# Optimization experiments

Hardware: AMD Instinct MI355X
Metric: run time of the kernel (lower is better)

Reference implementation:

```python
import jax, jax.numpy as jnp
import numpy as np


def setup_inputs() -> dict:
    key = jax.random.key(0)
    k1, k2, k3 = jax.random.split(key, 3)
    bs, seqlen, hidden = 2, 2048, 1024
    s, h = 4, 256  # sqrt_n_heads, head_size
    std = 0.02
    num_layers = 12
    hidden_states = jax.random.normal(k1, (bs, seqlen, hidden), dtype=jnp.float32)
    q_scale = 1.0 / np.sqrt(2.0 * num_layers * h)
    queries = jax.random.normal(k2, (s, h, h * s), dtype=jnp.float32) * std * q_scale
    combiners = jax.random.normal(k3, (s, h * s, h), dtype=jnp.float32) * (std * q_scale)
    return {"hidden_states": hidden_states, "queries": queries, "combiners": combiners}


def reference(hidden_states, queries, combiners):
    # queries: [s1, h, s*h], combiners: [s1, s*h, h]
    s, h, _ = queries.shape
    bs, S, E = hidden_states.shape
    x = hidden_states.reshape(bs, S, s, h)            # [b, t, s, h]
    qw = queries.reshape(s, h, s, h)                  # [s1, h_in, s2, h_out]
    # projected queries, already permuted to [s2, b, t, s1, f]
    Q = jnp.einsum('btae,aeqf->qbtaf', x, qw)
    # pre-attention scores: [s2, b, t, s1, u] (u = key position)  ~O(S^2)
    pre = jnp.einsum('qbtaf,buqf->qbtau', Q, x)
    # attention output, permuted to [s1, b, t, s2, g]
    attn = jnp.einsum('qbtau,buqg->abtqg', pre, x)
    attn = attn.reshape(s, bs, S, s * h)              # [s1, b, t, s2*h]
    out = jnp.einsum('abtk,akg->btag', attn, combiners)
    return out.reshape(bs, S, s * h)
```

## Files before the change

### kernel.cpp

```cpp
#include <hip/hip_runtime.h>
#include <hip/hip_bf16.h>


typedef unsigned short u16;
using short8  = __attribute__((ext_vector_type(8))) short;
using floatx4 = __attribute__((ext_vector_type(4))) float;

__device__ inline u16 f2bf(float f) {
    unsigned u = __float_as_uint(f);
    unsigned r = u + 0x7fffu + ((u >> 16) & 1u);
    return (u16)(r >> 16);
}

template <typename T>
__device__ inline void stage64(const T* __restrict__ src, long ld,
                               u16* __restrict__ dst, int tid) {
#pragma unroll
    for (int it = 0; it < 4; ++it) {
        const int flat = (it * 256 + tid) * 4;
        const int kl = flat & 63, rl = flat >> 6;
        ushort4 v;
        if (sizeof(T) == 4) {
            const float4 f = *(const float4*)&((const float*)src)[(long)rl * ld + kl];
            v.x = f2bf(f.x); v.y = f2bf(f.y); v.z = f2bf(f.z); v.w = f2bf(f.w);
        } else {
            v = *(const ushort4*)&((const u16*)src)[(long)rl * ld + kl];
        }
        const int chunk = ((kl >> 5) * 4 + (rl >> 4)) * 64 + ((kl >> 3) & 3) * 16 + (rl & 15);
        *(ushort4*)&dst[chunk * 8 + (kl & 7)] = v;
    }
}

__device__ inline void stage_km64(const float* __restrict__ src, long ld,
                                  u16* __restrict__ dst, int tid) {
#pragma unroll
    for (int it = 0; it < 4; ++it) {
        const int flat = (it * 256 + tid) * 4;
        const int m = flat & 63, k = flat >> 6;
        const float4 f = *(const float4*)&src[(long)k * ld + m];
        const int cb_ = ((k >> 5) * 4 + (m >> 4)) * 64 + ((k & 31) >> 3) * 16 + (m & 15);
        const int j = k & 7;
        dst[(cb_ + 0) * 8 + j] = f2bf(f.x);
        dst[(cb_ + 1) * 8 + j] = f2bf(f.y);
        dst[(cb_ + 2) * 8 + j] = f2bf(f.z);
        dst[(cb_ + 3) * 8 + j] = f2bf(f.w);
    }
}

template <typename TA, typename TB, bool AKM, bool BKM, bool ATOMIC>
__device__ inline void gemm_tile(const TA* __restrict__ A, long lda,
                                 const TB* __restrict__ B, long ldb,
                                 float* __restrict__ C, long ldc,
                                 int m0, int n0) {
    __shared__ u16 As[16384];
    __shared__ u16 Bs[16384];
    const int tid = threadIdx.x, lane = tid & 63, w = tid >> 6;
    const int IA = (w & 1) * 2, JB = (w >> 1) * 2;
    floatx4 acc[2][2] = {};

#pragma unroll
    for (int kb = 0; kb < 4; ++kb) {
        if (AKM) stage_km64((const float*)A + (long)(kb * 64) * lda, lda, As + kb * 4096, tid);
        else     stage64(A + kb * 64, lda, As + kb * 4096, tid);
    }
#pragma unroll
    for (int kb = 0; kb < 4; ++kb) {
        if (BKM) stage_km64((const float*)B + (long)(kb * 64) * ldb, ldb, Bs + kb * 4096, tid);
        else     stage64(B + kb * 64, ldb, Bs + kb * 4096, tid);
    }
    __syncthreads();

#pragma unroll
    for (int kb = 0; kb < 4; ++kb)
#pragma unroll
        for (int s = 0; s < 2; ++s) {
            short8 af[2], bfr[2];
#pragma unroll
            for (int i = 0; i < 2; ++i)
                af[i] = *(const short8*)&As[kb * 4096 + ((s * 4 + IA + i) * 64 + lane) * 8];
#pragma unroll
            for (int j = 0; j < 2; ++j)
                bfr[j] = *(const short8*)&Bs[kb * 4096 + ((s * 4 + JB + j) * 64 + lane) * 8];
#pragma unroll
            for (int i = 0; i < 2; ++i)
#pragma unroll
                for (int j = 0; j < 2; ++j)
                    acc[i][j] = __builtin_amdgcn_mfma_f32_16x16x32_bf16(af[i], bfr[j], acc[i][j], 0, 0, 0);
        }

    const int rb = (lane >> 4) * 4, col = lane & 15;
#pragma unroll
    for (int i = 0; i < 2; ++i)
#pragma unroll
        for (int j = 0; j < 2; ++j)
#pragma unroll
            for (int r = 0; r < 4; ++r) {
                const int gm = m0 + (IA + i) * 16 + rb + r;
                const int gn = n0 + (JB + j) * 16 + col;
                float* p = &C[(long)gm * ldc + gn];
                if (ATOMIC) atomicAdd(p, acc[i][j][r]); else *p = acc[i][j][r];
            }
}

__global__ __launch_bounds__(256) void k_gram(const float* __restrict__ x,
                                              float* __restrict__ G) {
    const int tile = blockIdx.x, bq = blockIdx.y, split = blockIdx.z;
    const int tm = tile >> 2, tn = tile & 3;
    const int b = bq >> 2, q = bq & 3;
    const float* base = x + (long)b * 2097152 + (long)split * 256 * 1024 + q * 256;
    gemm_tile<float, float, true, true, true>(
        base + tm * 64, 1024,
        base + tn * 64, 1024,
        G + (long)bq * 65536, 256,
        tm * 64, tn * 64);
}

__global__ __launch_bounds__(256) void k_2a(const float* __restrict__ comb,
                                            const float* __restrict__ G,
                                            float* __restrict__ Tt) {
    const int tile = blockIdx.x, i = blockIdx.y;
    const int tm = tile >> 2, tn = tile & 3;
    const int q = i & 3, ba = i >> 2, b = ba >> 2, a = ba & 3;
    gemm_tile<float, float, true, false, false>(
        comb + (long)a * 262144 + (long)q * 256 * 256 + tm * 64, 256,
        G + (long)(b * 4 + q) * 65536 + (long)tn * 64 * 256, 256,
        Tt + (long)ba * 262144, 1024,
        tm * 64, q * 256 + tn * 64);
}

__global__ __launch_bounds__(256) void k_2b(const float* __restrict__ Tt,
                                            const float* __restrict__ qw,
                                            float* __restrict__ Wt) {
    const int tile = blockIdx.x, ba = blockIdx.y, split = blockIdx.z;
    const int tm = tile >> 2, tn = tile & 3;
    const int a = ba & 3;
    gemm_tile<float, float, false, false, true>(
        Tt + (long)ba * 262144 + (long)tm * 64 * 1024 + split * 256, 1024,
        qw + (long)a * 262144 + (long)tn * 64 * 1024 + split * 256, 1024,
        Wt + (long)ba * 65536, 256,
        tm * 64, tn * 64);
}

__global__ __launch_bounds__(256) void k_3(const float* __restrict__ x,
                                           const float* __restrict__ Wt,
                                           float* __restrict__ out) {
    const int tl = blockIdx.x, ba = blockIdx.y;
    const int tm = tl >> 2, tn = tl & 3;
    const int b = ba >> 2, a = ba & 3;
    gemm_tile<float, float, false, false, false>(
        x + (long)b * 2097152 + (long)tm * 64 * 1024 + a * 256, 1024,
        Wt + (long)ba * 65536 + (long)tn * 64 * 256, 256,
        out + (long)b * 2097152 + a * 256, 1024,
        tm * 64, tn * 64);
}

extern "C" void kernel_launch(void* const* d_in, const int* in_sizes, int n_in,
                              void* d_out, int out_size, void* d_ws, size_t ws_size,
                              hipStream_t stream) {
    const float* x    = (const float*)d_in[0];
    const float* qw   = (const float*)d_in[1];
    const float* comb = (const float*)d_in[2];
    float* out = (float*)d_out;

    char* ws = (char*)d_ws;
    float* G  = (float*)(ws);
    float* Wt = (float*)(ws + (2u << 20));
    float* Tt = (float*)(ws + (4u << 20));

    hipMemsetAsync(d_ws, 0, 4u << 20, stream);
    k_gram<<<dim3(16, 8, 8), 256, 0, stream>>>(x, G);
    k_2a  <<<dim3(16, 32),   256, 0, stream>>>(comb, G, Tt);
    k_2b  <<<dim3(16, 8, 4), 256, 0, stream>>>(Tt, qw, Wt);
    k_3   <<<dim3(128, 8),   256, 0, stream>>>(x, Wt, out);
}
```

Baseline: 140.4 us.

## Replace atomic split-K Gram with partial buffers, fold zeroing, store Tt as bf16

The Gram kernel now writes per-split partial results to separate buffers instead of accumulating them with atomics. The next kernel sums the eight partials while staging its B operand. The separate memset is removed: the Gram kernel zeroes the Wt accumulator itself. Tt is stored as bf16, which halves its write and read traffic, at the cost of 8x more Gram partial storage and extra reads in k_2a.

```diff
diff --git a/kernel.cpp b/kernel.cpp
--- a/kernel.cpp
+++ b/kernel.cpp
@@ -26,6 +26,27 @@
         } else {
             v = *(const ushort4*)&((const u16*)src)[(long)rl * ld + kl];
         }
+        const int chunk = ((kl >> 5) * 4 + (rl >> 4)) * 64 + ((kl >> 3) & 3) * 16 + (rl & 15);
+        *(ushort4*)&dst[chunk * 8 + (kl & 7)] = v;
+    }
+}
+
+__device__ inline void stage64_sum8(const float* __restrict__ s0, long ld,
+                                    long partStride,
+                                    u16* __restrict__ dst, int tid) {
+#pragma unroll
+    for (int it = 0; it < 4; ++it) {
+        const int flat = (it * 256 + tid) * 4;
+        const int kl = flat & 63, rl = flat >> 6;
+        const long off = (long)rl * ld + kl;
+        float4 acc = *(const float4*)&s0[off];
+#pragma unroll
+        for (int s = 1; s < 8; ++s) {
+            const float4 f = *(const float4*)&s0[(long)s * partStride + off];
+            acc.x += f.x; acc.y += f.y; acc.z += f.z; acc.w += f.w;
+        }
+        ushort4 v;
+        v.x = f2bf(acc.x); v.y = f2bf(acc.y); v.z = f2bf(acc.z); v.w = f2bf(acc.w);
         const int chunk = ((kl >> 5) * 4 + (rl >> 4)) * 64 + ((kl >> 3) & 3) * 16 + (rl & 15);
         *(ushort4*)&dst[chunk * 8 + (kl & 7)] = v;
     }
@@ -47,10 +68,12 @@
     }
 }
 
-template <typename TA, typename TB, bool AKM, bool BKM, bool ATOMIC>
+template <typename TA, typename TB, typename TC,
+          bool AKM, bool BKM, bool BSUM8, bool ATOMIC>
 __device__ inline void gemm_tile(const TA* __restrict__ A, long lda,
                                  const TB* __restrict__ B, long ldb,
-                                 float* __restrict__ C, long ldc,
+                                 long partStride,
+                                 TC* __restrict__ C, long ldc,
                                  int m0, int n0) {
     __shared__ u16 As[16384];
     __shared__ u16 Bs[16384];
@@ -65,8 +88,9 @@
     }
 #pragma unroll
     for (int kb = 0; kb < 4; ++kb) {
-        if (BKM) stage_km64((const float*)B + (long)(kb * 64) * ldb, ldb, Bs + kb * 4096, tid);
-        else     stage64(B + kb * 64, ldb, Bs + kb * 4096, tid);
+        if (BSUM8)    stage64_sum8((const float*)B + kb * 64, ldb, partStride, Bs + kb * 4096, tid);
+        else if (BKM) stage_km64((const float*)B + (long)(kb * 64) * ldb, ldb, Bs + kb * 4096, tid);
+        else          stage64(B + kb * 64, ldb, Bs + kb * 4096, tid);
     }
     __syncthreads();
 
@@ -97,46 +121,57 @@
             for (int r = 0; r < 4; ++r) {
                 const int gm = m0 + (IA + i) * 16 + rb + r;
                 const int gn = n0 + (JB + j) * 16 + col;
-                float* p = &C[(long)gm * ldc + gn];
-                if (ATOMIC) atomicAdd(p, acc[i][j][r]); else *p = acc[i][j][r];
+                TC* p = &C[(long)gm * ldc + gn];
+                if (sizeof(TC) == 2) *(u16*)p = f2bf(acc[i][j][r]);
+                else if (ATOMIC) atomicAdd((float*)p, acc[i][j][r]);
+                else *(float*)p = acc[i][j][r];
             }
 }
 
 __global__ __launch_bounds__(256) void k_gram(const float* __restrict__ x,
-                                              float* __restrict__ G) {
+                                              float* __restrict__ Gp,
+                                              float* __restrict__ Wt) {
     const int tile = blockIdx.x, bq = blockIdx.y, split = blockIdx.z;
     const int tm = tile >> 2, tn = tile & 3;
     const int b = bq >> 2, q = bq & 3;
+    {
+        const int bl = tile + 16 * bq + 128 * split;
+        if (threadIdx.x < 128) {
+            const float4 zero = {0.f, 0.f, 0.f, 0.f};
+            ((float4*)(Wt + (long)bl * 512))[threadIdx.x] = zero;
+        }
+    }
     const float* base = x + (long)b * 2097152 + (long)split * 256 * 1024 + q * 256;
-    gemm_tile<float, float, true, true, true>(
+    gemm_tile<float, float, float, true, true, false, false>(
         base + tm * 64, 1024,
-        base + tn * 64, 1024,
-        G + (long)bq * 65536, 256,
+        base + tn * 64, 1024, 0,
+        Gp + (long)(split * 8 + bq) * 65536, 256,
         tm * 64, tn * 64);
 }
 
 __global__ __launch_bounds__(256) void k_2a(const float* __restrict__ comb,
-                                            const float* __restrict__ G,
-                                            float* __restrict__ Tt) {
+                                            const float* __restrict__ Gp,
+                                            u16* __restrict__ Tt) {
     const int tile = blockIdx.x, i = blockIdx.y;
     const int tm = tile >> 2, tn = tile & 3;
     const int q = i & 3, ba = i >> 2, b = ba >> 2, a = ba & 3;
-    gemm_tile<float, float, true, false, false>(
+    gemm_tile<float, float, u16, true, false, true, false>(
         comb + (long)a * 262144 + (long)q * 256 * 256 + tm * 64, 256,
-        G + (long)(b * 4 + q) * 65536 + (long)tn * 64 * 256, 256,
+        Gp + (long)(b * 4 + q) * 65536 + (long)tn * 64 * 256, 256,
+        (long)8 * 65536,
         Tt + (long)ba * 262144, 1024,
         tm * 64, q * 256 + tn * 64);
 }
 
-__global__ __launch_bounds__(256) void k_2b(const float* __restrict__ Tt,
+__global__ __launch_bounds__(256) void k_2b(const u16* __restrict__ Tt,
                                             const float* __restrict__ qw,
                                             float* __restrict__ Wt) {
     const int tile = blockIdx.x, ba = blockIdx.y, split = blockIdx.z;
     const int tm = tile >> 2, tn = tile & 3;
     const int a = ba & 3;
-    gemm_tile<float, float, false, false, true>(
+    gemm_tile<u16, float, float, false, false, false, true>(
         Tt + (long)ba * 262144 + (long)tm * 64 * 1024 + split * 256, 1024,
-        qw + (long)a * 262144 + (long)tn * 64 * 1024 + split * 256, 1024,
+        qw + (long)a * 262144 + (long)tn * 64 * 1024 + split * 256, 1024, 0,
         Wt + (long)ba * 65536, 256,
         tm * 64, tn * 64);
 }
@@ -147,9 +182,9 @@
     const int tl = blockIdx.x, ba = blockIdx.y;
     const int tm = tl >> 2, tn = tl & 3;
     const int b = ba >> 2, a = ba & 3;
-    gemm_tile<float, float, false, false, false>(
+    gemm_tile<float, float, float, false, false, false, false>(
         x + (long)b * 2097152 + (long)tm * 64 * 1024 + a * 256, 1024,
-        Wt + (long)ba * 65536 + (long)tn * 64 * 256, 256,
+        Wt + (long)ba * 65536 + (long)tn * 64 * 256, 256, 0,
         out + (long)b * 2097152 + a * 256, 1024,
         tm * 64, tn * 64);
 }
@@ -163,13 +198,12 @@
     float* out = (float*)d_out;
 
     char* ws = (char*)d_ws;
-    float* G  = (float*)(ws);
-    float* Wt = (float*)(ws + (2u << 20));
-    float* Tt = (float*)(ws + (4u << 20));
-
-    hipMemsetAsync(d_ws, 0, 4u << 20, stream);
-    k_gram<<<dim3(16, 8, 8), 256, 0, stream>>>(x, G);
-    k_2a  <<<dim3(16, 32),   256, 0, stream>>>(comb, G, Tt);
+    float* Gp = (float*)(ws);
+    float* Wt = (float*)(ws + (16u << 20));
+    u16*   Tt = (u16*)  (ws + (18u << 20));
+
+    k_gram<<<dim3(16, 8, 8), 256, 0, stream>>>(x, Gp, Wt);
+    k_2a  <<<dim3(16, 32),   256, 0, stream>>>(comb, Gp, Tt);
     k_2b  <<<dim3(16, 8, 4), 256, 0, stream>>>(Tt, qw, Wt);
     k_3   <<<dim3(128, 8),   256, 0, stream>>>(x, Wt, out);
 }
```

Result: no change. 138.1 us (-1.6%).
